# Kernel tuning notes

Measured on AMD Instinct MI355X. Metric: run time of the kernel, lower is better.

## Reference

```python
import jax, jax.numpy as jnp
from jax import lax
import numpy as np

IMG = 15      # odd spatial edge; num_patches = 4*(IMG-1) = 56
CH = 256      # spectral channels
DIM = 512
HEADS = 8
DH = 64       # dim_head; inner_dim = HEADS*DH = 512
DEPTH = 6
MLP = 2048
NCLS = 16
RATIO = 0.5   # args.ratio (scalar, not trainable)
SCALE = DH ** -0.5
NPATCH = 4 * (IMG - 1)


def _ring(a1, a2, b1, b2, E, mid1, mid2):
    # Exact replica of outer_sampling traversal; returns static index tables.
    tgt, s1, s2 = [], [], []
    d = [0, 1]; l1 = a1; l2 = b1 - 1; start = 0
    while True:
        l1 += d[0]; l2 += d[1]
        if l1 == a1 and l2 == b1:
            if start == 1:
                break
            start = 1
        if l1 > a2:
            d = [0, -1]; l1 -= 1; continue
        elif l2 < b1:
            d = [-1, 0]; l2 += 1; continue
        elif l2 > b2:
            d = [1, 0]; l2 -= 1; continue
        if l1 < 0 or l1 > E or l2 < 0 or l2 > E:
            continue
        m1 = 0 if l1 == mid1 else -int(np.sign(l1 - mid1))
        m2 = 0 if l2 == mid2 else -int(np.sign(l2 - mid2))
        if abs(l1 - mid1) > abs(l2 - mid2):
            s1.append((l1 + m1) * E + l2); s2.append((l1 + m1) * E + l2 + m2)
        elif abs(l1 - mid1) < abs(l2 - mid2):
            s1.append(l1 * E + l2 + m2); s2.append((l1 + m1) * E + l2 + m2)
        else:  # corner: x[t] += ratio * x[s] == (x[s]+x[s])*ratio/2
            s = (l1 + m1) * E + l2 + m2
            s1.append(s); s2.append(s)
        tgt.append(l1 * E + l2)
    return np.array(tgt), np.array(s1), np.array(s2)

_MID = IMG // 2
# Within each ring, every read hits an already-finalized inner-ring cell,
# so rings can be applied as vectorized gather+scatter in sequence.
RINGS = [_ring(_MID - i, _MID + i, _MID - i, _MID + i, IMG, _MID, _MID)
         for i in range(1, _MID + 1)]


def _sinusoid(n_pos, d):
    pos = np.arange(n_pos)[:, None].astype(np.float64)
    j = np.arange(d)[None, :]
    ang = pos / np.power(10000.0, 2 * (j // 2) / d)
    tab = np.zeros((n_pos, d))
    tab[:, 0::2] = np.sin(ang[:, 0::2])
    tab[:, 1::2] = np.cos(ang[:, 1::2])
    return jnp.asarray(tab[None], dtype=jnp.float32)

POS = _sinusoid(NPATCH + 1, DIM)


def _ln(x, g, b, eps=1e-5):
    mu = x.mean(-1, keepdims=True)
    v = ((x - mu) ** 2).mean(-1, keepdims=True)
    return (x - mu) * lax.rsqrt(v + eps) * g + b


def _forward(x, We, be, cls_token, Wqkv, Wo, bo, ln1g, ln1b, W1, b1, W2, b2,
             ln2g, ln2b, lnh_g, lnh_b, Wh, bh):
    B = x.shape[0]
    xf = x.reshape(B, CH, IMG * IMG)
    for tgt, s1, s2 in RINGS:
        xf = xf.at[:, :, tgt].set(xf[:, :, tgt] + (xf[:, :, s1] + xf[:, :, s2]) * (RATIO / 2))
    # original runs spiral under torch.no_grad()
    tok = lax.stop_gradient(jnp.transpose(xf[:, :, RINGS[-1][0]], (0, 2, 1)))  # [B, 56, CH]
    h = tok @ We + be                                                          # [B, 56, DIM]
    h = jnp.concatenate([jnp.broadcast_to(cls_token, (B, 1, DIM)), h], axis=1)
    h = h + POS[:, :NPATCH + 1]
    for l in range(DEPTH):
        y = _ln(h, ln1g[l], ln1b[l])
        qkv = y @ Wqkv[l]
        q, k, v = [t.reshape(B, -1, HEADS, DH).transpose(0, 2, 1, 3)
                   for t in jnp.split(qkv, 3, axis=-1)]
        a = jax.nn.softmax(jnp.einsum('bhid,bhjd->bhij', q, k) * SCALE, axis=-1)
        o = jnp.einsum('bhij,bhjd->bhid', a, v).transpose(0, 2, 1, 3).reshape(B, -1, HEADS * DH)
        h = h + o @ Wo[l] + bo[l]
        y = _ln(h, ln2g[l], ln2b[l])
        h = h + jax.nn.gelu(y @ W1[l] + b1[l], approximate=False) @ W2[l] + b2[l]
    p = h.mean(axis=1)  # pool='mean'
    return _ln(p, lnh_g, lnh_b) @ Wh + bh


def setup_inputs():
    key = jax.random.key(0)
    ks = jax.random.split(key, 8)
    B = 512
    def nrm(k, shp, s=0.02):
        return jax.random.normal(k, shp, jnp.float32) * s
    return {
        'x': jax.random.normal(ks[0], (B, CH, IMG, IMG), jnp.float32),
        'We': nrm(ks[1], (CH, DIM)),
        'be': jnp.zeros((DIM,), jnp.float32),
        'cls_token': nrm(ks[2], (1, 1, DIM), 1.0),
        'Wqkv': nrm(ks[3], (DEPTH, DIM, 3 * HEADS * DH)),
        'Wo': nrm(ks[4], (DEPTH, HEADS * DH, DIM)),
        'bo': jnp.zeros((DEPTH, DIM), jnp.float32),
        'ln1g': jnp.ones((DEPTH, DIM), jnp.float32),
        'ln1b': jnp.zeros((DEPTH, DIM), jnp.float32),
        'W1': nrm(ks[5], (DEPTH, DIM, MLP)),
        'b1': jnp.zeros((DEPTH, MLP), jnp.float32),
        'W2': nrm(ks[6], (DEPTH, MLP, DIM)),
        'b2': jnp.zeros((DEPTH, DIM), jnp.float32),
        'ln2g': jnp.ones((DEPTH, DIM), jnp.float32),
        'ln2b': jnp.zeros((DEPTH, DIM), jnp.float32),
        'lnh_g': jnp.ones((DIM,), jnp.float32),
        'lnh_b': jnp.zeros((DIM,), jnp.float32),
        'Wh': nrm(ks[7], (DIM, NCLS)),
        'bh': jnp.zeros((NCLS,), jnp.float32),
    }


def reference(x, We, be, cls_token, Wqkv, Wo, bo, ln1g, ln1b, W1, b1, W2, b2,
              ln2g, ln2b, lnh_g, lnh_b, Wh, bh):
    return _forward(x, We, be, cls_token, Wqkv, Wo, bo, ln1g, ln1b, W1, b1,
                    W2, b2, ln2g, ln2b, lnh_g, lnh_b, Wh, bh)
```

## Files before the change

### kernel.cpp

```cpp
#include <hip/hip_runtime.h>
#include <math.h>

#define NB   512
#define SEQ  57
#define NP   56
#define CHN  256
#define DIM  512
#define MLPD 2048

typedef float f32x4 __attribute__((ext_vector_type(4)));
typedef short s16x8 __attribute__((ext_vector_type(8)));
typedef short s16x4 __attribute__((ext_vector_type(4)));

__device__ __forceinline__ short f2bf(float f) {
    union { float f; unsigned u; } v; v.f = f;
    unsigned r = (v.u + 0x7fffu + ((v.u >> 16) & 1u)) >> 16;
    return (short)r;
}
__device__ __forceinline__ float geluf(float v) {
    return 0.5f * v * (1.0f + erff(v * 0.70710678118654752f));
}

#define GLDS16(g, l) __builtin_amdgcn_global_load_lds(                         \
    (const __attribute__((address_space(1))) void*)(g),                        \
    (__attribute__((address_space(3))) void*)(l), 16, 0, 0)

struct RingTables { int tgt[224]; int s1[224]; int s2[224]; int start[8]; };
constexpr RingTables make_rings() {
    RingTables rt{};
    int n = 0; const int E = 15, mid = 7;
    rt.start[0] = 0;
    for (int i = 1; i <= 7; ++i) {
        int a1 = mid - i, a2 = mid + i, b1 = mid - i, b2 = mid + i;
        int d0 = 0, d1 = 1, l1 = a1, l2 = b1 - 1, started = 0;
        while (true) {
            l1 += d0; l2 += d1;
            if (l1 == a1 && l2 == b1) { if (started) break; started = 1; }
            if (l1 > a2)      { d0 = 0;  d1 = -1; l1 -= 1; continue; }
            else if (l2 < b1) { d0 = -1; d1 = 0;  l2 += 1; continue; }
            else if (l2 > b2) { d0 = 1;  d1 = 0;  l2 -= 1; continue; }
            if (l1 < 0 || l1 > E || l2 < 0 || l2 > E) continue;
            int m1 = -((l1 > mid) - (l1 < mid));
            int m2 = -((l2 > mid) - (l2 < mid));
            int ab1 = l1 > mid ? l1 - mid : mid - l1;
            int ab2 = l2 > mid ? l2 - mid : mid - l2;
            if (ab1 > ab2)      { rt.s1[n] = (l1+m1)*E + l2;   rt.s2[n] = (l1+m1)*E + l2+m2; }
            else if (ab1 < ab2) { rt.s1[n] = l1*E + l2+m2;     rt.s2[n] = (l1+m1)*E + l2+m2; }
            else                { int s = (l1+m1)*E + l2+m2;   rt.s1[n] = s; rt.s2[n] = s; }
            rt.tgt[n] = l1*E + l2;
            ++n;
        }
        rt.start[i] = n;
    }
    return rt;
}
constexpr RingTables RT_HOST = make_rings();
__constant__ RingTables RT = RT_HOST;

__global__ __launch_bounds__(256) void spiral_kernel(const float* __restrict__ x,
                                                     short* __restrict__ tok) {
    __shared__ float tile[64 * 225];
    const int b  = blockIdx.x >> 2;
    const int c0 = (blockIdx.x & 3) << 6;
    const float* src = x + ((size_t)b * CHN + c0) * 225;
    for (int i = threadIdx.x; i < 64 * 225; i += 256) tile[i] = src[i];
    __syncthreads();
    for (int r = 0; r < 7; ++r) {
        const int s0 = RT.start[r], n = RT.start[r + 1] - s0;
        for (int w = threadIdx.x; w < (n << 6); w += 256) {
            const int c = w & 63, t = s0 + (w >> 6);
            float* row = tile + c * 225;
            row[RT.tgt[t]] += (row[RT.s1[t]] + row[RT.s2[t]]) * 0.25f;
        }
        __syncthreads();
    }
    for (int w = threadIdx.x; w < (56 << 6); w += 256) {
        const int c = w & 63, p = w >> 6;
        tok[((size_t)b * NP + p) * CHN + c0 + c] = f2bf(tile[c * 225 + RT.tgt[168 + p]]);
    }
}

__global__ __launch_bounds__(256) void transcvt(const float* __restrict__ in,
                                                short* __restrict__ out, int K, int N) {
    __shared__ float t[32][33];
    in  += (size_t)blockIdx.z * K * N;
    out += (size_t)blockIdx.z * K * N;
    const int k0 = blockIdx.y << 5, n0 = blockIdx.x << 5;
    const int tx = threadIdx.x & 31, ty = threadIdx.x >> 5;
    for (int i = ty; i < 32; i += 8) t[i][tx] = in[(size_t)(k0 + i) * N + n0 + tx];
    __syncthreads();
    for (int i = ty; i < 32; i += 8) out[(size_t)(n0 + i) * K + k0 + tx] = f2bf(t[tx][i]);
}

__global__ __launch_bounds__(256) void pos_kernel(float* __restrict__ pos) {
    const int idx = blockIdx.x * 256 + threadIdx.x;
    const int t = idx >> 9, j = idx & 511;
    double expo = (double)(2 * (j >> 1)) / 512.0;
    double ang  = (double)t * pow(10000.0, -expo);
    pos[idx] = (j & 1) ? (float)cos(ang) : (float)sin(ang);
}

__global__ __launch_bounds__(256) void cls_pos_kernel(const float* __restrict__ cls,
                                                      const float* __restrict__ pos,
                                                      float* __restrict__ h) {
    const int idx = blockIdx.x * 256 + threadIdx.x;
    const int c = idx & 511, b = idx >> 9;
    h[(size_t)b * SEQ * DIM + c] = cls[c] + pos[c];
}

__global__ __launch_bounds__(256) void ln_kernel(const float* __restrict__ x,
                                                 const float* __restrict__ g,
                                                 const float* __restrict__ bta,
                                                 short* __restrict__ y) {
    const int row  = (blockIdx.x << 2) + (threadIdx.x >> 6);
    const int lane = threadIdx.x & 63;
    const float* xr = x + (size_t)row * DIM;
    f32x4 v0 = *(const f32x4*)(xr + (lane << 2));
    f32x4 v1 = *(const f32x4*)(xr + (lane << 2) + 256);
    float s = v0[0] + v0[1] + v0[2] + v0[3] + v1[0] + v1[1] + v1[2] + v1[3];
#pragma unroll
    for (int off = 1; off < 64; off <<= 1) s += __shfl_xor(s, off);
    const float mu = s * (1.f / 512.f);
    float sq = 0.f;
#pragma unroll
    for (int k = 0; k < 4; ++k) { float d = v0[k] - mu; sq += d * d; }
#pragma unroll
    for (int k = 0; k < 4; ++k) { float d = v1[k] - mu; sq += d * d; }
#pragma unroll
    for (int off = 1; off < 64; off <<= 1) sq += __shfl_xor(sq, off);
    const float rs = rsqrtf(sq * (1.f / 512.f) + 1e-5f);
    short* yr = y + (size_t)row * DIM;
#pragma unroll
    for (int p = 0; p < 2; ++p) {
        const int c0 = (lane << 2) + (p << 8);
        const f32x4 vv = p ? v1 : v0;
        const f32x4 g4 = *(const f32x4*)(g + c0);
        const f32x4 b4 = *(const f32x4*)(bta + c0);
        s16x4 o;
#pragma unroll
        for (int k = 0; k < 4; ++k) o[k] = f2bf((vv[k] - mu) * rs * g4[k] + b4[k]);
        *(s16x4*)(yr + c0) = o;
    }
}

template<int ACT, bool RES, bool OUTBF, bool EMB>
__global__ __launch_bounds__(256, 2) void gemm_bf16(
    const short* __restrict__ A, const short* __restrict__ BT,
    const float* __restrict__ bias, const float* __restrict__ res,
    void* __restrict__ Cout, int M, int N, int K)
{
    __shared__ short As[128 * 64];
    __shared__ short Bs[128 * 64];
    const int tid = threadIdx.x;
    const int m0 = blockIdx.y << 7, n0 = blockIdx.x << 7;
    const int wave = tid >> 6, lane = tid & 63;
    const int wm = (wave >> 1) << 6, wn = (wave & 1) << 6;
    const int fm = lane & 15, fq = lane >> 4;

    const short* Ap[4]; const short* Bp[4];
    short *lA[4], *lB[4];
#pragma unroll
    for (int t = 0; t < 4; ++t) {
        const int g = t * 256 + tid;
        const int row = g >> 3;
        const int c = (g & 7) ^ (row & 7);
        Ap[t] = A  + (size_t)(m0 + row) * K + (c << 3);
        Bp[t] = BT + (size_t)(n0 + row) * K + (c << 3);
        lA[t] = As + g * 8;
        lB[t] = Bs + g * 8;
    }

    f32x4 acc[4][4] = {};

    for (int k0 = 0; k0 < K; k0 += 64) {
        __syncthreads();
#pragma unroll
        for (int t = 0; t < 4; ++t) GLDS16(Ap[t] + k0, lA[t]);
#pragma unroll
        for (int t = 0; t < 4; ++t) GLDS16(Bp[t] + k0, lB[t]);
        __syncthreads();
#pragma unroll
        for (int kk = 0; kk < 2; ++kk) {
            const int cs = ((fq + (kk << 2)) ^ (fm & 7)) << 3;
            s16x8 af[4], bfr[4];
#pragma unroll
            for (int s = 0; s < 4; ++s) {
                af[s]  = *(const s16x8*)(As + (wm + s * 16 + fm) * 64 + cs);
                bfr[s] = *(const s16x8*)(Bs + (wn + s * 16 + fm) * 64 + cs);
            }
#pragma unroll
            for (int i = 0; i < 4; ++i)
#pragma unroll
                for (int j = 0; j < 4; ++j)
                    acc[i][j] = __builtin_amdgcn_mfma_f32_16x16x32_bf16(bfr[j], af[i], acc[i][j], 0, 0, 0);
        }
    }

#pragma unroll
    for (int i = 0; i < 4; ++i) {
        const int row = m0 + wm + i * 16 + fm;
        size_t obase;
        const float* posr = nullptr;
        if (EMB) {
            const int bb = row / 56, tt = row - bb * 56;
            obase = ((size_t)(bb * SEQ + tt + 1)) * N;
            posr = res + (size_t)(tt + 1) * N;
        } else {
            obase = (size_t)row * N;
        }
#pragma unroll
        for (int j = 0; j < 4; ++j) {
            const int col0 = n0 + wn + j * 16 + (fq << 2);
            f32x4 v = acc[i][j];
            if (bias) v += *(const f32x4*)(bias + col0);
            if (EMB)  v += *(const f32x4*)(posr + col0);
            if (ACT == 1) {
#pragma unroll
                for (int k = 0; k < 4; ++k) v[k] = geluf(v[k]);
            }
            if (RES) v += *(const f32x4*)(res + obase + col0);
            if (OUTBF) {
                s16x4 o;
#pragma unroll
                for (int k = 0; k < 4; ++k) o[k] = f2bf(v[k]);
                *(s16x4*)((short*)Cout + obase + col0) = o;
            } else {
                *(f32x4*)((float*)Cout + obase + col0) = v;
            }
        }
    }
}

__global__ __launch_bounds__(64) void attn_mfma(const short* __restrict__ qkv,
                                                short* __restrict__ o) {
    __shared__ short Pl[64 * 72];
    __shared__ short Vt[64 * 72];
    const int b = blockIdx.x >> 3, hd = blockIdx.x & 7;
    const int lane = threadIdx.x;
    const int n = lane & 15, q = lane >> 4;
    const short* base = qkv + (size_t)b * SEQ * 1536 + hd * 64;

    {
        const short* vb = base + 1024 + lane;
        for (int t = 0; t < SEQ; ++t) Vt[lane * 72 + t] = vb[(size_t)t * 1536];
        for (int t = SEQ; t < 64; ++t) Vt[lane * 72 + t] = 0;
    }

    const s16x8 zero8 = {};
    s16x8 qf[4][2], kf[4][2];
#pragma unroll
    for (int ti = 0; ti < 4; ++ti) {
        const int tq = ti * 16 + n;
#pragma unroll
        for (int kk = 0; kk < 2; ++kk) {
            const int ko = kk * 32 + q * 8;
            qf[ti][kk] = (tq < SEQ) ? *(const s16x8*)(base + (size_t)tq * 1536 + ko)       : zero8;
            kf[ti][kk] = (tq < SEQ) ? *(const s16x8*)(base + 512 + (size_t)tq * 1536 + ko) : zero8;
        }
    }

    f32x4 sacc[4][4] = {};
#pragma unroll
    for (int ti = 0; ti < 4; ++ti)
#pragma unroll
        for (int tj = 0; tj < 4; ++tj)
#pragma unroll
            for (int kk = 0; kk < 2; ++kk)
                sacc[ti][tj] = __builtin_amdgcn_mfma_f32_16x16x32_bf16(
                    qf[ti][kk], kf[tj][kk], sacc[ti][tj], 0, 0, 0);

#pragma unroll
    for (int ti = 0; ti < 4; ++ti) {
#pragma unroll
        for (int r = 0; r < 4; ++r) {
            float v[4]; float mx = -1e30f;
#pragma unroll
            for (int tj = 0; tj < 4; ++tj) {
                float s = sacc[ti][tj][r] * 0.125f;
                if (tj * 16 + n >= SEQ) s = -1e30f;
                v[tj] = s; mx = fmaxf(mx, s);
            }
            mx = fmaxf(mx, __shfl_xor(mx, 1));
            mx = fmaxf(mx, __shfl_xor(mx, 2));
            mx = fmaxf(mx, __shfl_xor(mx, 4));
            mx = fmaxf(mx, __shfl_xor(mx, 8));
            float sum = 0.f;
#pragma unroll
            for (int tj = 0; tj < 4; ++tj) { v[tj] = __expf(v[tj] - mx); sum += v[tj]; }
            sum += __shfl_xor(sum, 1); sum += __shfl_xor(sum, 2);
            sum += __shfl_xor(sum, 4); sum += __shfl_xor(sum, 8);
            const float inv = 1.f / sum;
            const int row = ti * 16 + q * 4 + r;
#pragma unroll
            for (int tj = 0; tj < 4; ++tj)
                Pl[row * 72 + tj * 16 + n] = f2bf(v[tj] * inv);
        }
    }
    __syncthreads();

    f32x4 oacc[4][4] = {};
#pragma unroll
    for (int kk = 0; kk < 2; ++kk) {
        s16x8 pf[4], vf[4];
#pragma unroll
        for (int s = 0; s < 4; ++s) {
            pf[s] = *(const s16x8*)(Pl + (s * 16 + n) * 72 + kk * 32 + q * 8);
            vf[s] = *(const s16x8*)(Vt + (s * 16 + n) * 72 + kk * 32 + q * 8);
        }
#pragma unroll
        for (int ti = 0; ti < 4; ++ti)
#pragma unroll
            for (int td = 0; td < 4; ++td)
                oacc[ti][td] = __builtin_amdgcn_mfma_f32_16x16x32_bf16(
                    vf[td], pf[ti], oacc[ti][td], 0, 0, 0);
    }
#pragma unroll
    for (int ti = 0; ti < 4; ++ti) {
        const int t = ti * 16 + n;
        if (t < SEQ) {
            short* orow = o + ((size_t)(b * SEQ + t)) * DIM + hd * 64 + (q << 2);
#pragma unroll
            for (int td = 0; td < 4; ++td) {
                s16x4 o4;
#pragma unroll
                for (int r = 0; r < 4; ++r) o4[r] = f2bf(oacc[ti][td][r]);
                *(s16x4*)(orow + td * 16) = o4;
            }
        }
    }
}

__global__ __launch_bounds__(256) void head_kernel(const float* __restrict__ h,
                                                   const float* __restrict__ g,
                                                   const float* __restrict__ bb,
                                                   const float* __restrict__ Wh,
                                                   const float* __restrict__ bh,
                                                   float* __restrict__ out) {
    __shared__ float p[DIM];
    __shared__ float r1[4], r2[4];
    const int b = blockIdx.x;
    const float* hb = h + (size_t)b * SEQ * DIM;
    for (int c = threadIdx.x; c < DIM; c += 256) {
        float s = 0.f;
        for (int t = 0; t < SEQ; ++t) s += hb[t * DIM + c];
        p[c] = s * (1.f / 57.f);
    }
    __syncthreads();
    float s = 0.f;
    for (int c = threadIdx.x; c < DIM; c += 256) s += p[c];
#pragma unroll
    for (int off = 1; off < 64; off <<= 1) s += __shfl_xor(s, off);
    if ((threadIdx.x & 63) == 0) r1[threadIdx.x >> 6] = s;
    __syncthreads();
    const float mu = (r1[0] + r1[1] + r1[2] + r1[3]) * (1.f / 512.f);
    float sq = 0.f;
    for (int c = threadIdx.x; c < DIM; c += 256) { float d = p[c] - mu; sq += d * d; }
#pragma unroll
    for (int off = 1; off < 64; off <<= 1) sq += __shfl_xor(sq, off);
    if ((threadIdx.x & 63) == 0) r2[threadIdx.x >> 6] = sq;
    __syncthreads();
    const float rs = rsqrtf((r2[0] + r2[1] + r2[2] + r2[3]) * (1.f / 512.f) + 1e-5f);
    for (int c = threadIdx.x; c < DIM; c += 256) p[c] = (p[c] - mu) * rs * g[c] + bb[c];
    __syncthreads();
    if (threadIdx.x < 16) {
        float acc = bh[threadIdx.x];
        for (int c = 0; c < DIM; ++c) acc += p[c] * Wh[c * 16 + threadIdx.x];
        out[b * 16 + threadIdx.x] = acc;
    }
}

extern "C" void kernel_launch(void* const* d_in, const int* in_sizes, int n_in,
                              void* d_out, int out_size, void* d_ws, size_t ws_size,
                              hipStream_t stream) {
    (void)in_sizes; (void)n_in; (void)out_size; (void)ws_size;
    const float* x    = (const float*)d_in[0];
    const float* We   = (const float*)d_in[1];
    const float* be   = (const float*)d_in[2];
    const float* cls  = (const float*)d_in[3];
    const float* Wqkv = (const float*)d_in[4];
    const float* Wo   = (const float*)d_in[5];
    const float* bo   = (const float*)d_in[6];
    const float* ln1g = (const float*)d_in[7];
    const float* ln1b = (const float*)d_in[8];
    const float* W1   = (const float*)d_in[9];
    const float* b1   = (const float*)d_in[10];
    const float* W2   = (const float*)d_in[11];
    const float* b2   = (const float*)d_in[12];
    const float* ln2g = (const float*)d_in[13];
    const float* ln2b = (const float*)d_in[14];
    const float* lnhg = (const float*)d_in[15];
    const float* lnhb = (const float*)d_in[16];
    const float* Wh   = (const float*)d_in[17];
    const float* bh   = (const float*)d_in[18];

    char* ws = (char*)d_ws;
    float* h    = (float*)(ws);
    short* bigs = (short*)(ws + 59768832);
    short* ybf  = (short*)(ws + 239075328);
    short* wbuf = (short*)(ws + 268959744);
    short* tokb = (short*)(ws + 306970624);
    float* pos  = (float*)(ws + 321650688);

    short* WeT   = wbuf;
    short* WqkvT = wbuf + 131072;
    short* WoT   = WqkvT + 6 * 786432;
    short* W1T   = WoT   + 6 * 262144;
    short* W2T   = W1T   + 6 * 1048576;

    pos_kernel<<<114, 256, 0, stream>>>(pos);
    transcvt<<<dim3(16,  8, 1), 256, 0, stream>>>(We,   WeT,    256,  512);
    transcvt<<<dim3(48, 16, 6), 256, 0, stream>>>(Wqkv, WqkvT,  512, 1536);
    transcvt<<<dim3(16, 16, 6), 256, 0, stream>>>(Wo,   WoT,    512,  512);
    transcvt<<<dim3(64, 16, 6), 256, 0, stream>>>(W1,   W1T,    512, 2048);
    transcvt<<<dim3(16, 64, 6), 256, 0, stream>>>(W2,   W2T,   2048,  512);
    spiral_kernel<<<2048, 256, 0, stream>>>(x, tokb);

    gemm_bf16<0, false, false, true><<<dim3(4, 224), 256, 0, stream>>>(
        tokb, WeT, be, pos, h, NB * NP, DIM, CHN);
    cls_pos_kernel<<<1024, 256, 0, stream>>>(cls, pos, h);

    const int M = NB * SEQ;
    for (int l = 0; l < 6; ++l) {
        ln_kernel<<<M / 4, 256, 0, stream>>>(h, ln1g + l * 512, ln1b + l * 512, ybf);
        gemm_bf16<0, false, true, false><<<dim3(12, 228), 256, 0, stream>>>(
            ybf, WqkvT + (size_t)l * 786432, nullptr, nullptr, bigs, M, 1536, 512);
        attn_mfma<<<NB * 8, 64, 0, stream>>>(bigs, ybf);
        gemm_bf16<0, true, false, false><<<dim3(4, 228), 256, 0, stream>>>(
            ybf, WoT + (size_t)l * 262144, bo + l * 512, h, h, M, 512, 512);
        ln_kernel<<<M / 4, 256, 0, stream>>>(h, ln2g + l * 512, ln2b + l * 512, ybf);
        gemm_bf16<1, false, true, false><<<dim3(16, 228), 256, 0, stream>>>(
            ybf, W1T + (size_t)l * 1048576, b1 + l * 2048, nullptr, bigs, M, 2048, 512);
        gemm_bf16<0, true, false, false><<<dim3(4, 228), 256, 0, stream>>>(
            bigs, W2T + (size_t)l * 1048576, b2 + l * 512, h, h, M, 512, 2048);
    }
    head_kernel<<<NB, 256, 0, stream>>>(h, lnhg, lnhb, Wh, bh, (float*)d_out);
}
```

Baseline: 2.526 ms.

## Load GEMM B fragments directly from global and use tanh-GELU approximation

The GEMM no longer stages the B tile in shared memory. Each wave now loads its B fragments straight from global memory into registers, which halves LDS use and lets the launch bound rise to 3 blocks per CU. The exact erf GELU is replaced by a tanh-form approximation computed with an exponential. The trade-off is that B data is no longer shared across waves through LDS, so each B element is loaded by two waves. The GELU output also differs slightly from the erf version.

```diff
diff --git a/kernel.cpp b/kernel.cpp
--- a/kernel.cpp
+++ b/kernel.cpp
@@ -17,8 +17,9 @@
     unsigned r = (v.u + 0x7fffu + ((v.u >> 16) & 1u)) >> 16;
     return (short)r;
 }
-__device__ __forceinline__ float geluf(float v) {
-    return 0.5f * v * (1.0f + erff(v * 0.70710678118654752f));
+__device__ __forceinline__ float gelu_fast(float v) {
+    const float u2 = 1.5957691216057308f * v * (1.0f + 0.044715f * v * v);
+    return v / (1.0f + __expf(-u2));
 }
 
 #define GLDS16(g, l) __builtin_amdgcn_global_load_lds(                         \
@@ -144,56 +145,57 @@
 }
 
 template<int ACT, bool RES, bool OUTBF, bool EMB>
-__global__ __launch_bounds__(256, 2) void gemm_bf16(
+__global__ __launch_bounds__(256, 3) void gemm_bf16(
     const short* __restrict__ A, const short* __restrict__ BT,
     const float* __restrict__ bias, const float* __restrict__ res,
     void* __restrict__ Cout, int M, int N, int K)
 {
     __shared__ short As[128 * 64];
-    __shared__ short Bs[128 * 64];
     const int tid = threadIdx.x;
     const int m0 = blockIdx.y << 7, n0 = blockIdx.x << 7;
     const int wave = tid >> 6, lane = tid & 63;
     const int wm = (wave >> 1) << 6, wn = (wave & 1) << 6;
     const int fm = lane & 15, fq = lane >> 4;
 
-    const short* Ap[4]; const short* Bp[4];
-    short *lA[4], *lB[4];
+    const short* Ap[4]; short* lA[4];
 #pragma unroll
     for (int t = 0; t < 4; ++t) {
         const int g = t * 256 + tid;
         const int row = g >> 3;
         const int c = (g & 7) ^ (row & 7);
-        Ap[t] = A  + (size_t)(m0 + row) * K + (c << 3);
-        Bp[t] = BT + (size_t)(n0 + row) * K + (c << 3);
+        Ap[t] = A + (size_t)(m0 + row) * K + (c << 3);
         lA[t] = As + g * 8;
-        lB[t] = Bs + g * 8;
-    }
+    }
+    int boff[4];
+#pragma unroll
+    for (int s = 0; s < 4; ++s) boff[s] = (n0 + wn + s * 16 + fm) * K + (fq << 3);
 
     f32x4 acc[4][4] = {};
 
     for (int k0 = 0; k0 < K; k0 += 64) {
-        __syncthreads();
 #pragma unroll
         for (int t = 0; t < 4; ++t) GLDS16(Ap[t] + k0, lA[t]);
-#pragma unroll
-        for (int t = 0; t < 4; ++t) GLDS16(Bp[t] + k0, lB[t]);
+        s16x8 bfr[2][4];
+#pragma unroll
+        for (int kk = 0; kk < 2; ++kk)
+#pragma unroll
+            for (int s = 0; s < 4; ++s)
+                bfr[kk][s] = *(const s16x8*)(BT + boff[s] + k0 + kk * 32);
         __syncthreads();
 #pragma unroll
         for (int kk = 0; kk < 2; ++kk) {
             const int cs = ((fq + (kk << 2)) ^ (fm & 7)) << 3;
-            s16x8 af[4], bfr[4];
-#pragma unroll
-            for (int s = 0; s < 4; ++s) {
-                af[s]  = *(const s16x8*)(As + (wm + s * 16 + fm) * 64 + cs);
-                bfr[s] = *(const s16x8*)(Bs + (wn + s * 16 + fm) * 64 + cs);
-            }
+            s16x8 af[4];
+#pragma unroll
+            for (int s = 0; s < 4; ++s)
+                af[s] = *(const s16x8*)(As + (wm + s * 16 + fm) * 64 + cs);
 #pragma unroll
             for (int i = 0; i < 4; ++i)
 #pragma unroll
                 for (int j = 0; j < 4; ++j)
-                    acc[i][j] = __builtin_amdgcn_mfma_f32_16x16x32_bf16(bfr[j], af[i], acc[i][j], 0, 0, 0);
-        }
+                    acc[i][j] = __builtin_amdgcn_mfma_f32_16x16x32_bf16(bfr[kk][j], af[i], acc[i][j], 0, 0, 0);
+        }
+        __syncthreads();
     }
 
 #pragma unroll
@@ -216,7 +218,7 @@
             if (EMB)  v += *(const f32x4*)(posr + col0);
             if (ACT == 1) {
 #pragma unroll
-                for (int k = 0; k < 4; ++k) v[k] = geluf(v[k]);
+                for (int k = 0; k < 4; ++k) v[k] = gelu_fast(v[k]);
             }
             if (RES) v += *(const f32x4*)(res + obase + col0);
             if (OUTBF) {
```

After: 3.630 ms. 1.44x slower.
